# Optimization experiments

Measured on AMD Instinct MI355X. Metric: run time of the kernel, lower is better.

The kernel has to match this reference:

```python
import jax, jax.numpy as jnp
import numpy as np

B, S, H, NH = 2, 2048, 1024, 16


def setup_inputs() -> dict:
    key = jax.random.key(0)
    ks = jax.random.split(key, 5)
    x = jax.random.normal(ks[0], (B, S, H), dtype=jnp.float32)
    # causal mask: True = attend
    mask = jnp.tril(jnp.ones((S, S), dtype=bool))[None, None, :, :]
    scale = 1.0 / np.sqrt(H)
    Wq = jax.random.normal(ks[1], (H, H), dtype=jnp.float32) * scale
    Wk = jax.random.normal(ks[2], (H, H), dtype=jnp.float32) * scale
    Wv = jax.random.normal(ks[3], (H, H), dtype=jnp.float32) * scale
    Wo = jax.random.normal(ks[4], (H, H), dtype=jnp.float32) * scale
    return {"x": x, "mask": mask, "Wq": Wq, "Wk": Wk, "Wv": Wv, "Wo": Wo}


def _split_heads(t, n_heads):
    b, s, h = t.shape
    return t.reshape(b, s, n_heads, h // n_heads).transpose(0, 2, 1, 3)  # (b,h,s,d)


def reference(x, mask, Wq, Wk, Wv, Wo):
    q = _split_heads(x @ Wq, NH)
    k = _split_heads(x @ Wk, NH)
    v = _split_heads(x @ Wv, NH)
    d_head = q.shape[-1]
    scores = jnp.einsum('bhqd,bhkd->bhqk', q, k) / jnp.sqrt(jnp.asarray(d_head, q.dtype))
    neg = jnp.asarray(jnp.finfo(scores.dtype).min, scores.dtype)
    scores = jnp.where(mask, scores, neg)  # mask_to_bias: True->0 bias, False->-inf
    attn = jax.nn.softmax(scores, axis=-1)
    out = jnp.einsum('bhqk,bhkd->bhqd', attn, v)
    out = out.transpose(0, 2, 1, 3).reshape(x.shape[0], x.shape[1], -1)  # merge heads
    return out @ Wo
```

## Files before the change

kernel.cpp:

```cpp
#include <hip/hip_runtime.h>

using u16 = unsigned short;
typedef __attribute__((ext_vector_type(8))) __bf16 bf16x8;
typedef __attribute__((ext_vector_type(4))) float f32x4;
typedef __attribute__((ext_vector_type(8))) u16 u16x8;
typedef __attribute__((ext_vector_type(4))) u16 u16x4;
typedef __attribute__((ext_vector_type(4))) float floatx4;

__device__ __forceinline__ u16 f2bf(float f) {
    union { float f; unsigned u; } x; x.f = f;
    unsigned r = x.u + 0x7fffu + ((x.u >> 16) & 1u);
    return (u16)(r >> 16);
}

__device__ __forceinline__ void gload16(const void* g, void* l) {
    __builtin_amdgcn_global_load_lds((const __attribute__((address_space(1))) void*)g,
                                     (__attribute__((address_space(3))) void*)l, 16, 0, 0);
}

constexpr int Hdim = 1024, Bdim = 2, Sdim = 2048, Dh = 64;
constexpr int NTOK = Bdim * Sdim;

__global__ void cast_x_kernel(const float* __restrict__ x, u16* __restrict__ xb, int n4) {
    int i = blockIdx.x * blockDim.x + threadIdx.x;
    int stride = gridDim.x * blockDim.x;
    for (; i < n4; i += stride) {
        floatx4 v = reinterpret_cast<const floatx4*>(x)[i];
        u16x4 o;
        #pragma unroll
        for (int j = 0; j < 4; ++j) o[j] = f2bf(v[j]);
        reinterpret_cast<u16x4*>(xb)[i] = o;
    }
}

__global__ void transpose_cast_w(const float* __restrict__ W0, const float* __restrict__ W1,
                                 const float* __restrict__ W2, const float* __restrict__ W3,
                                 u16* __restrict__ T0, u16* __restrict__ T1,
                                 u16* __restrict__ T2, u16* __restrict__ T3) {
    __shared__ float tile[32][33];
    const float* W; u16* T;
    switch (blockIdx.z) {
        case 0: W = W0; T = T0; break;
        case 1: W = W1; T = T1; break;
        case 2: W = W2; T = T2; break;
        default: W = W3; T = T3; break;
    }
    int bx = blockIdx.x * 32, by = blockIdx.y * 32;
    int tx = threadIdx.x, ty = threadIdx.y;
    #pragma unroll
    for (int i = 0; i < 4; ++i)
        tile[ty + i * 8][tx] = W[(size_t)(by + ty + i * 8) * Hdim + bx + tx];
    __syncthreads();
    #pragma unroll
    for (int i = 0; i < 4; ++i)
        T[(size_t)(bx + ty + i * 8) * Hdim + by + tx] = f2bf(tile[tx][ty + i * 8]);
}

template <int MODE, int BN>
__global__ __launch_bounds__(256) void gemm_bt(const u16* __restrict__ A, const u16* __restrict__ Bt,
                                               void* __restrict__ C0, void* __restrict__ C1,
                                               void* __restrict__ C2, int N, int K) {
    constexpr int NB = BN / 32;
    __shared__ __align__(16) u16 As[128 * 32];
    __shared__ __align__(16) u16 Bs[BN * 32];
    const int tid = threadIdx.x;
    const int lane = tid & 63, wid = tid >> 6;
    const int wr = wid >> 1, wc = wid & 1;
    const int fr = lane & 15, g = lane >> 4, k8 = g * 8;
    const int rowBase = blockIdx.y * 128, colBase = blockIdx.x * BN;
    const int sr = lane >> 2, sc = (lane & 3) * 8;
    f32x4 acc[4][NB] = {};
    for (int k0 = 0; k0 < K; k0 += 32) {
        __syncthreads();
        #pragma unroll
        for (int i = 0; i < 2; ++i) {
            const int rb = wid * 32 + i * 16;
            gload16(&A[(size_t)(rowBase + rb + sr) * K + k0 + sc], &As[rb * 32]);
        }
        if constexpr (BN == 128) {
            #pragma unroll
            for (int i = 0; i < 2; ++i) {
                const int rb = wid * 32 + i * 16;
                gload16(&Bt[(size_t)(colBase + rb + sr) * K + k0 + sc], &Bs[rb * 32]);
            }
        } else {
            const int rb = wid * 16;
            gload16(&Bt[(size_t)(colBase + rb + sr) * K + k0 + sc], &Bs[rb * 32]);
        }
        __syncthreads();
        bf16x8 af[4], bfr[NB];
        #pragma unroll
        for (int m = 0; m < 4; ++m)
            af[m] = *reinterpret_cast<const bf16x8*>(&As[(wr * 64 + m * 16 + fr) * 32 + k8]);
        #pragma unroll
        for (int n = 0; n < NB; ++n)
            bfr[n] = *reinterpret_cast<const bf16x8*>(&Bs[(wc * (BN / 2) + n * 16 + fr) * 32 + k8]);
        #pragma unroll
        for (int m = 0; m < 4; ++m)
            #pragma unroll
            for (int n = 0; n < NB; ++n)
                acc[m][n] = __builtin_amdgcn_mfma_f32_16x16x32_bf16(af[m], bfr[n], acc[m][n], 0, 0, 0);
    }
    #pragma unroll
    for (int m = 0; m < 4; ++m) {
        #pragma unroll
        for (int n = 0; n < NB; ++n) {
            const int row = rowBase + wr * 64 + m * 16 + g * 4;
            const int col = colBase + wc * (BN / 2) + n * 16 + fr;
            if constexpr (MODE == 0) {
                u16* C = (u16*)C0;
                #pragma unroll
                for (int j = 0; j < 4; ++j) C[(size_t)(row + j) * N + col] = f2bf(acc[m][n][j]);
            } else if constexpr (MODE == 1) {
                float* C = (float*)C0;
                #pragma unroll
                for (int j = 0; j < 4; ++j) C[(size_t)(row + j) * N + col] = acc[m][n][j];
            } else {
                if (col < 1024) {
                    u16* Qm = (u16*)C0;
                    #pragma unroll
                    for (int j = 0; j < 4; ++j) Qm[(size_t)(row + j) * 1024 + col] = f2bf(acc[m][n][j]);
                } else if (col < 2048) {
                    u16* Km = (u16*)C1;
                    #pragma unroll
                    for (int j = 0; j < 4; ++j) Km[(size_t)(row + j) * 1024 + (col - 1024)] = f2bf(acc[m][n][j]);
                } else {
                    u16* Vt = (u16*)C2;
                    u16x4 pk;
                    #pragma unroll
                    for (int j = 0; j < 4; ++j) pk[j] = f2bf(acc[m][n][j]);
                    *reinterpret_cast<u16x4*>(&Vt[(size_t)(col - 2048) * NTOK + row]) = pk;
                }
            }
        }
    }
}

__global__ __launch_bounds__(256, 2) void attn_kernel(const u16* __restrict__ Q, const u16* __restrict__ Km,
                                                      const u16* __restrict__ VtG, u16* __restrict__ AO) {
    __shared__ __align__(16) u16 Kt[2][64 * 64];
    __shared__ __align__(16) u16 Vt[2][64 * 64];
    __shared__ __align__(16) u16 Pw[4][32][72];
    const int tid = threadIdx.x, lane = tid & 63, w = tid >> 6;
    const int bid = blockIdx.x;
    const int xg = bid & 7, rem = bid >> 3;
    const int p = rem & 15, yg = rem >> 4;
    const int grp = xg + 8 * yg;
    const int h = grp & 15, b = grp >> 4;
    const int qsel[2] = { p, 31 - p };
    const int h0 = h * Dh;
    const size_t boff = (size_t)b * Sdim * Hdim;
    const u16* Qb = Q + boff;
    u16* AOb = AO + boff;
    const int fr = lane & 15, g = lane >> 4;

    const int lr = lane >> 3;
    const int lc8 = ((lane & 7) ^ lr) * 8;
    const u16* Kg = Km + boff + (size_t)(w * 8 + lr) * Hdim + h0 + lc8;
    const u16* Vg = VtG + (size_t)(h0 + w * 8 + lr) * NTOK + (size_t)b * Sdim + lc8;

    auto stage = [&](int t, int bufi) {
        const int kv0 = t * 64;
        #pragma unroll
        for (int i = 0; i < 2; ++i) {
            gload16(Kg + (size_t)(kv0 + i * 32) * Hdim, &Kt[bufi][w * 512 + i * 2048]);
            gload16(Vg + (size_t)(i * 32) * NTOK + kv0, &Vt[bufi][w * 512 + i * 2048]);
        }
    };

    constexpr float QSCALE = 0.125f * 1.44269504089f;
    bf16x8 qf[2][2];
    int qrow0[2];
    #pragma unroll
    for (int m = 0; m < 2; ++m) {
        qrow0[m] = qsel[m] * 64 + w * 16;
        #pragma unroll
        for (int c = 0; c < 2; ++c) {
            bf16x8 t = *reinterpret_cast<const bf16x8*>(
                &Qb[(size_t)(qrow0[m] + fr) * Hdim + h0 + c * 32 + g * 8]);
            bf16x8 r;
            #pragma unroll
            for (int j = 0; j < 8; ++j) r[j] = (__bf16)((float)t[j] * QSCALE);
            qf[m][c] = r;
        }
    }

    f32x4 o[2][4] = {};
    float mrow[2][4], lrow[2][4];
    #pragma unroll
    for (int m = 0; m < 2; ++m)
        #pragma unroll
        for (int j = 0; j < 4; ++j) { mrow[m][j] = -INFINITY; lrow[m][j] = 0.f; }

    const int ntiles = qsel[1] + 1;
    stage(0, 0);
    __syncthreads();
    int buf = 0;
    for (int t = 0; t < ntiles; ++t) {
        if (t + 1 < ntiles) stage(t + 1, buf ^ 1);
        const int kv0 = t * 64;
        #pragma unroll
        for (int m = 0; m < 2; ++m) {
            if (t > qsel[m]) continue;
            const bool masked = (t == qsel[m]);
            f32x4 s[4];
            __builtin_amdgcn_s_setprio(1);
            #pragma unroll
            for (int n = 0; n < 4; ++n) {
                const int row = n * 16 + fr;
                const int sw = (row & 7) << 3;
                const u16* kp = &Kt[buf][row * 64];
                bf16x8 kf0 = *reinterpret_cast<const bf16x8*>(&kp[(g * 8) ^ sw]);
                bf16x8 kf1 = *reinterpret_cast<const bf16x8*>(&kp[(32 + g * 8) ^ sw]);
                f32x4 z = {};
                z = __builtin_amdgcn_mfma_f32_16x16x32_bf16(qf[m][0], kf0, z, 0, 0, 0);
                s[n] = __builtin_amdgcn_mfma_f32_16x16x32_bf16(qf[m][1], kf1, z, 0, 0, 0);
            }
            __builtin_amdgcn_s_setprio(0);
            #pragma unroll
            for (int j = 0; j < 4; ++j) {
                const int qrow = qrow0[m] + g * 4 + j;
                float mx = -3.0e38f;
                #pragma unroll
                for (int n = 0; n < 4; ++n) {
                    float v = s[n][j];
                    if (masked) {
                        int kv = kv0 + n * 16 + fr;
                        v = (kv <= qrow) ? v : -3.0e38f;
                        s[n][j] = v;
                    }
                    mx = fmaxf(mx, v);
                }
                #pragma unroll
                for (int off = 1; off < 16; off <<= 1) mx = fmaxf(mx, __shfl_xor(mx, off));
                const float mnew = fmaxf(mrow[m][j], mx);
                const float alpha = exp2f(mrow[m][j] - mnew);
                float rs = 0.f;
                #pragma unroll
                for (int n = 0; n < 4; ++n) {
                    float pv = exp2f(s[n][j] - mnew);
                    rs += pv;
                    Pw[w][m * 16 + g * 4 + j][n * 16 + fr] = f2bf(pv);
                }
                #pragma unroll
                for (int off = 1; off < 16; off <<= 1) rs += __shfl_xor(rs, off);
                lrow[m][j] = lrow[m][j] * alpha + rs;
                mrow[m][j] = mnew;
                #pragma unroll
                for (int n = 0; n < 4; ++n) o[m][n][j] *= alpha;
            }
            bf16x8 pa0 = *reinterpret_cast<const bf16x8*>(&Pw[w][m * 16 + fr][g * 8]);
            bf16x8 pa1 = *reinterpret_cast<const bf16x8*>(&Pw[w][m * 16 + fr][32 + g * 8]);
            __builtin_amdgcn_s_setprio(1);
            #pragma unroll
            for (int n = 0; n < 4; ++n) {
                const int row = n * 16 + fr;
                const int sw = (row & 7) << 3;
                const u16* vp = &Vt[buf][row * 64];
                bf16x8 vf0 = *reinterpret_cast<const bf16x8*>(&vp[(g * 8) ^ sw]);
                bf16x8 vf1 = *reinterpret_cast<const bf16x8*>(&vp[(32 + g * 8) ^ sw]);
                o[m][n] = __builtin_amdgcn_mfma_f32_16x16x32_bf16(pa0, vf0, o[m][n], 0, 0, 0);
                o[m][n] = __builtin_amdgcn_mfma_f32_16x16x32_bf16(pa1, vf1, o[m][n], 0, 0, 0);
            }
            __builtin_amdgcn_s_setprio(0);
        }
        __syncthreads();
        buf ^= 1;
    }

    #pragma unroll
    for (int m = 0; m < 2; ++m) {
        float invl[4];
        #pragma unroll
        for (int j = 0; j < 4; ++j) invl[j] = 1.0f / lrow[m][j];
        #pragma unroll
        for (int n = 0; n < 4; ++n)
            #pragma unroll
            for (int j = 0; j < 4; ++j) {
                int qrow = qrow0[m] + g * 4 + j;
                AOb[(size_t)qrow * Hdim + h0 + n * 16 + fr] = f2bf(o[m][n][j] * invl[j]);
            }
    }
}

extern "C" void kernel_launch(void* const* d_in, const int* in_sizes, int n_in,
                              void* d_out, int out_size, void* d_ws, size_t ws_size,
                              hipStream_t stream) {
    const float* x  = (const float*)d_in[0];
    const float* Wq = (const float*)d_in[2];
    const float* Wk = (const float*)d_in[3];
    const float* Wv = (const float*)d_in[4];
    const float* Wo = (const float*)d_in[5];
    float* out = (float*)d_out;

    u16* ws  = (u16*)d_ws;
    u16* Xb  = ws;
    u16* WqT = ws  + 4194304;
    u16* WkT = WqT + 1048576;
    u16* WvT = WkT + 1048576;
    u16* WoT = WvT + 1048576;
    u16* Qm  = WoT + 1048576;
    u16* Km  = Qm  + 4194304;
    u16* Vt  = Km  + 4194304;
    u16* AO  = Vt  + 4194304;

    cast_x_kernel<<<2048, 256, 0, stream>>>(x, Xb, NTOK * Hdim / 4);
    transpose_cast_w<<<dim3(32, 32, 4), dim3(32, 8), 0, stream>>>(Wq, Wk, Wv, Wo, WqT, WkT, WvT, WoT);
    gemm_bt<2, 128><<<dim3(24, 32), 256, 0, stream>>>(Xb, WqT, Qm, Km, Vt, 3072, Hdim);
    attn_kernel<<<dim3(512), 256, 0, stream>>>(Qm, Km, Vt, AO);
    gemm_bt<1, 64><<<dim3(16, 32), 256, 0, stream>>>(AO, WoT, out, nullptr, nullptr, Hdim, Hdim);
}
```

Measured before the change: 231.5 us.

## Retile attention to one q-tile per block, deepen GEMM K-step, lazy softmax rescale

The attention kernel now gives each block a single 64-row query tile instead of a balanced pair, doubling the grid to 1024 blocks, raising the occupancy hint to 3 and shrinking the P scratch buffer. It also skips the online-softmax rescale when the new row max stays within a threshold of the old one. The GEMM loads 64-wide K slices per barrier instead of 32, halving synchronisation count, and bf16 conversion switches to the compiler cast. Risks include causal load imbalance from dropping the paired tiles, larger LDS use in the GEMM, and the lazy rescale letting exponentials exceed one before normalisation.

```diff
diff --git a/kernel.cpp b/kernel.cpp
--- a/kernel.cpp
+++ b/kernel.cpp
@@ -7,10 +7,9 @@
 typedef __attribute__((ext_vector_type(4))) u16 u16x4;
 typedef __attribute__((ext_vector_type(4))) float floatx4;
 
-__device__ __forceinline__ u16 f2bf(float f) {
-    union { float f; unsigned u; } x; x.f = f;
-    unsigned r = x.u + 0x7fffu + ((x.u >> 16) & 1u);
-    return (u16)(r >> 16);
+__device__ __forceinline__ u16 f2b(float f) {
+    __bf16 h = (__bf16)f;
+    return __builtin_bit_cast(u16, h);
 }
 
 __device__ __forceinline__ void gload16(const void* g, void* l) {
@@ -28,7 +27,7 @@
         floatx4 v = reinterpret_cast<const floatx4*>(x)[i];
         u16x4 o;
         #pragma unroll
-        for (int j = 0; j < 4; ++j) o[j] = f2bf(v[j]);
+        for (int j = 0; j < 4; ++j) o[j] = f2b(v[j]);
         reinterpret_cast<u16x4*>(xb)[i] = o;
     }
 }
@@ -53,7 +52,7 @@
     __syncthreads();
     #pragma unroll
     for (int i = 0; i < 4; ++i)
-        T[(size_t)(bx + ty + i * 8) * Hdim + by + tx] = f2bf(tile[tx][ty + i * 8]);
+        T[(size_t)(bx + ty + i * 8) * Hdim + by + tx] = f2b(tile[tx][ty + i * 8]);
 }
 
 template <int MODE, int BN>
@@ -61,45 +60,43 @@
                                                void* __restrict__ C0, void* __restrict__ C1,
                                                void* __restrict__ C2, int N, int K) {
     constexpr int NB = BN / 32;
-    __shared__ __align__(16) u16 As[128 * 32];
-    __shared__ __align__(16) u16 Bs[BN * 32];
+    __shared__ __align__(16) u16 As[128 * 64];
+    __shared__ __align__(16) u16 Bs[BN * 64];
     const int tid = threadIdx.x;
     const int lane = tid & 63, wid = tid >> 6;
     const int wr = wid >> 1, wc = wid & 1;
-    const int fr = lane & 15, g = lane >> 4, k8 = g * 8;
+    const int fr = lane & 15, g = lane >> 4;
     const int rowBase = blockIdx.y * 128, colBase = blockIdx.x * BN;
-    const int sr = lane >> 2, sc = (lane & 3) * 8;
+    const int sr = lane >> 3, sc = (lane & 7) * 8;
     f32x4 acc[4][NB] = {};
-    for (int k0 = 0; k0 < K; k0 += 32) {
+    for (int k0 = 0; k0 < K; k0 += 64) {
         __syncthreads();
         #pragma unroll
-        for (int i = 0; i < 2; ++i) {
-            const int rb = wid * 32 + i * 16;
-            gload16(&A[(size_t)(rowBase + rb + sr) * K + k0 + sc], &As[rb * 32]);
-        }
-        if constexpr (BN == 128) {
-            #pragma unroll
-            for (int i = 0; i < 2; ++i) {
-                const int rb = wid * 32 + i * 16;
-                gload16(&Bt[(size_t)(colBase + rb + sr) * K + k0 + sc], &Bs[rb * 32]);
-            }
-        } else {
-            const int rb = wid * 16;
-            gload16(&Bt[(size_t)(colBase + rb + sr) * K + k0 + sc], &Bs[rb * 32]);
+        for (int i = 0; i < 4; ++i) {
+            const int rb = i * 32 + wid * 8;
+            gload16(&A[(size_t)(rowBase + rb + sr) * K + k0 + sc], &As[rb * 64]);
+        }
+        #pragma unroll
+        for (int i = 0; i < BN / 32; ++i) {
+            const int rb = i * 32 + wid * 8;
+            gload16(&Bt[(size_t)(colBase + rb + sr) * K + k0 + sc], &Bs[rb * 64]);
         }
         __syncthreads();
-        bf16x8 af[4], bfr[NB];
-        #pragma unroll
-        for (int m = 0; m < 4; ++m)
-            af[m] = *reinterpret_cast<const bf16x8*>(&As[(wr * 64 + m * 16 + fr) * 32 + k8]);
-        #pragma unroll
-        for (int n = 0; n < NB; ++n)
-            bfr[n] = *reinterpret_cast<const bf16x8*>(&Bs[(wc * (BN / 2) + n * 16 + fr) * 32 + k8]);
-        #pragma unroll
-        for (int m = 0; m < 4; ++m)
+        #pragma unroll
+        for (int kk = 0; kk < 2; ++kk) {
+            bf16x8 af[4], bfr[NB];
+            #pragma unroll
+            for (int m = 0; m < 4; ++m)
+                af[m] = *reinterpret_cast<const bf16x8*>(&As[(wr * 64 + m * 16 + fr) * 64 + kk * 32 + g * 8]);
             #pragma unroll
             for (int n = 0; n < NB; ++n)
-                acc[m][n] = __builtin_amdgcn_mfma_f32_16x16x32_bf16(af[m], bfr[n], acc[m][n], 0, 0, 0);
+                bfr[n] = *reinterpret_cast<const bf16x8*>(&Bs[(wc * (BN / 2) + n * 16 + fr) * 64 + kk * 32 + g * 8]);
+            #pragma unroll
+            for (int m = 0; m < 4; ++m)
+                #pragma unroll
+                for (int n = 0; n < NB; ++n)
+                    acc[m][n] = __builtin_amdgcn_mfma_f32_16x16x32_bf16(af[m], bfr[n], acc[m][n], 0, 0, 0);
+        }
     }
     #pragma unroll
     for (int m = 0; m < 4; ++m) {
@@ -110,7 +107,7 @@
             if constexpr (MODE == 0) {
                 u16* C = (u16*)C0;
                 #pragma unroll
-                for (int j = 0; j < 4; ++j) C[(size_t)(row + j) * N + col] = f2bf(acc[m][n][j]);
+                for (int j = 0; j < 4; ++j) C[(size_t)(row + j) * N + col] = f2b(acc[m][n][j]);
             } else if constexpr (MODE == 1) {
                 float* C = (float*)C0;
                 #pragma unroll
@@ -119,16 +116,16 @@
                 if (col < 1024) {
                     u16* Qm = (u16*)C0;
                     #pragma unroll
-                    for (int j = 0; j < 4; ++j) Qm[(size_t)(row + j) * 1024 + col] = f2bf(acc[m][n][j]);
+                    for (int j = 0; j < 4; ++j) Qm[(size_t)(row + j) * 1024 + col] = f2b(acc[m][n][j]);
                 } else if (col < 2048) {
                     u16* Km = (u16*)C1;
                     #pragma unroll
-                    for (int j = 0; j < 4; ++j) Km[(size_t)(row + j) * 1024 + (col - 1024)] = f2bf(acc[m][n][j]);
+                    for (int j = 0; j < 4; ++j) Km[(size_t)(row + j) * 1024 + (col - 1024)] = f2b(acc[m][n][j]);
                 } else {
                     u16* Vt = (u16*)C2;
                     u16x4 pk;
                     #pragma unroll
-                    for (int j = 0; j < 4; ++j) pk[j] = f2bf(acc[m][n][j]);
+                    for (int j = 0; j < 4; ++j) pk[j] = f2b(acc[m][n][j]);
                     *reinterpret_cast<u16x4*>(&Vt[(size_t)(col - 2048) * NTOK + row]) = pk;
                 }
             }
@@ -136,23 +133,24 @@
     }
 }
 
-__global__ __launch_bounds__(256, 2) void attn_kernel(const u16* __restrict__ Q, const u16* __restrict__ Km,
+__global__ __launch_bounds__(256, 3) void attn_kernel(const u16* __restrict__ Q, const u16* __restrict__ Km,
                                                       const u16* __restrict__ VtG, u16* __restrict__ AO) {
     __shared__ __align__(16) u16 Kt[2][64 * 64];
     __shared__ __align__(16) u16 Vt[2][64 * 64];
-    __shared__ __align__(16) u16 Pw[4][32][72];
+    __shared__ __align__(16) u16 Pw[4][16][72];
     const int tid = threadIdx.x, lane = tid & 63, w = tid >> 6;
     const int bid = blockIdx.x;
     const int xg = bid & 7, rem = bid >> 3;
-    const int p = rem & 15, yg = rem >> 4;
+    const int qi = rem & 31, yg = rem >> 5;
     const int grp = xg + 8 * yg;
     const int h = grp & 15, b = grp >> 4;
-    const int qsel[2] = { p, 31 - p };
+    const int qb = 31 - qi;
     const int h0 = h * Dh;
     const size_t boff = (size_t)b * Sdim * Hdim;
     const u16* Qb = Q + boff;
     u16* AOb = AO + boff;
     const int fr = lane & 15, g = lane >> 4;
+    const int qrow0 = qb * 64 + w * 16;
 
     const int lr = lane >> 3;
     const int lc8 = ((lane & 7) ^ lr) * 8;
@@ -169,118 +167,109 @@
     };
 
     constexpr float QSCALE = 0.125f * 1.44269504089f;
-    bf16x8 qf[2][2];
-    int qrow0[2];
-    #pragma unroll
-    for (int m = 0; m < 2; ++m) {
-        qrow0[m] = qsel[m] * 64 + w * 16;
-        #pragma unroll
-        for (int c = 0; c < 2; ++c) {
-            bf16x8 t = *reinterpret_cast<const bf16x8*>(
-                &Qb[(size_t)(qrow0[m] + fr) * Hdim + h0 + c * 32 + g * 8]);
-            bf16x8 r;
-            #pragma unroll
-            for (int j = 0; j < 8; ++j) r[j] = (__bf16)((float)t[j] * QSCALE);
-            qf[m][c] = r;
-        }
-    }
-
-    f32x4 o[2][4] = {};
-    float mrow[2][4], lrow[2][4];
-    #pragma unroll
-    for (int m = 0; m < 2; ++m)
-        #pragma unroll
-        for (int j = 0; j < 4; ++j) { mrow[m][j] = -INFINITY; lrow[m][j] = 0.f; }
-
-    const int ntiles = qsel[1] + 1;
+    bf16x8 qf[2];
+    #pragma unroll
+    for (int c = 0; c < 2; ++c) {
+        bf16x8 t = *reinterpret_cast<const bf16x8*>(
+            &Qb[(size_t)(qrow0 + fr) * Hdim + h0 + c * 32 + g * 8]);
+        bf16x8 r;
+        #pragma unroll
+        for (int j = 0; j < 8; ++j) r[j] = (__bf16)((float)t[j] * QSCALE);
+        qf[c] = r;
+    }
+
+    f32x4 o[4] = {};
+    float mrow[4], lrow[4];
+    #pragma unroll
+    for (int j = 0; j < 4; ++j) { mrow[j] = -INFINITY; lrow[j] = 0.f; }
+
+    const int ntiles = qb + 1;
     stage(0, 0);
     __syncthreads();
     int buf = 0;
     for (int t = 0; t < ntiles; ++t) {
         if (t + 1 < ntiles) stage(t + 1, buf ^ 1);
         const int kv0 = t * 64;
-        #pragma unroll
-        for (int m = 0; m < 2; ++m) {
-            if (t > qsel[m]) continue;
-            const bool masked = (t == qsel[m]);
-            f32x4 s[4];
-            __builtin_amdgcn_s_setprio(1);
+        const bool masked = (t == qb);
+        f32x4 s[4];
+        __builtin_amdgcn_s_setprio(1);
+        #pragma unroll
+        for (int n = 0; n < 4; ++n) {
+            const int row = n * 16 + fr;
+            const int sw = (row & 7) << 3;
+            const u16* kp = &Kt[buf][row * 64];
+            bf16x8 kf0 = *reinterpret_cast<const bf16x8*>(&kp[(g * 8) ^ sw]);
+            bf16x8 kf1 = *reinterpret_cast<const bf16x8*>(&kp[(32 + g * 8) ^ sw]);
+            f32x4 z = {};
+            z = __builtin_amdgcn_mfma_f32_16x16x32_bf16(qf[0], kf0, z, 0, 0, 0);
+            s[n] = __builtin_amdgcn_mfma_f32_16x16x32_bf16(qf[1], kf1, z, 0, 0, 0);
+        }
+        __builtin_amdgcn_s_setprio(0);
+        #pragma unroll
+        for (int j = 0; j < 4; ++j) {
+            const int qrow = qrow0 + g * 4 + j;
+            float mx = -3.0e38f;
             #pragma unroll
             for (int n = 0; n < 4; ++n) {
-                const int row = n * 16 + fr;
-                const int sw = (row & 7) << 3;
-                const u16* kp = &Kt[buf][row * 64];
-                bf16x8 kf0 = *reinterpret_cast<const bf16x8*>(&kp[(g * 8) ^ sw]);
-                bf16x8 kf1 = *reinterpret_cast<const bf16x8*>(&kp[(32 + g * 8) ^ sw]);
-                f32x4 z = {};
-                z = __builtin_amdgcn_mfma_f32_16x16x32_bf16(qf[m][0], kf0, z, 0, 0, 0);
-                s[n] = __builtin_amdgcn_mfma_f32_16x16x32_bf16(qf[m][1], kf1, z, 0, 0, 0);
+                float v = s[n][j];
+                if (masked) {
+                    int kv = kv0 + n * 16 + fr;
+                    v = (kv <= qrow) ? v : -3.0e38f;
+                    s[n][j] = v;
+                }
+                mx = fmaxf(mx, v);
             }
-            __builtin_amdgcn_s_setprio(0);
-            #pragma unroll
-            for (int j = 0; j < 4; ++j) {
-                const int qrow = qrow0[m] + g * 4 + j;
-                float mx = -3.0e38f;
+            #pragma unroll
+            for (int off = 1; off < 16; off <<= 1) mx = fmaxf(mx, __shfl_xor(mx, off));
+            const bool skip = (__all(mx <= mrow[j] + 8.0f) != 0);
+            const float mnew = skip ? mrow[j] : fmaxf(mrow[j], mx);
+            float rs = 0.f;
+            #pragma unroll
+            for (int n = 0; n < 4; ++n) {
+                float pv = exp2f(s[n][j] - mnew);
+                rs += pv;
+                Pw[w][g * 4 + j][n * 16 + fr] = f2b(pv);
+            }
+            #pragma unroll
+            for (int off = 1; off < 16; off <<= 1) rs += __shfl_xor(rs, off);
+            if (skip) {
+                lrow[j] += rs;
+            } else {
+                const float alpha = exp2f(mrow[j] - mnew);
+                lrow[j] = lrow[j] * alpha + rs;
+                mrow[j] = mnew;
                 #pragma unroll
-                for (int n = 0; n < 4; ++n) {
-                    float v = s[n][j];
-                    if (masked) {
-                        int kv = kv0 + n * 16 + fr;
-                        v = (kv <= qrow) ? v : -3.0e38f;
-                        s[n][j] = v;
-                    }
-                    mx = fmaxf(mx, v);
-                }
-                #pragma unroll
-                for (int off = 1; off < 16; off <<= 1) mx = fmaxf(mx, __shfl_xor(mx, off));
-                const float mnew = fmaxf(mrow[m][j], mx);
-                const float alpha = exp2f(mrow[m][j] - mnew);
-                float rs = 0.f;
-                #pragma unroll
-                for (int n = 0; n < 4; ++n) {
-                    float pv = exp2f(s[n][j] - mnew);
-                    rs += pv;
-                    Pw[w][m * 16 + g * 4 + j][n * 16 + fr] = f2bf(pv);
-                }
-                #pragma unroll
-                for (int off = 1; off < 16; off <<= 1) rs += __shfl_xor(rs, off);
-                lrow[m][j] = lrow[m][j] * alpha + rs;
-                mrow[m][j] = mnew;
-                #pragma unroll
-                for (int n = 0; n < 4; ++n) o[m][n][j] *= alpha;
+                for (int n = 0; n < 4; ++n) o[n][j] *= alpha;
             }
-            bf16x8 pa0 = *reinterpret_cast<const bf16x8*>(&Pw[w][m * 16 + fr][g * 8]);
-            bf16x8 pa1 = *reinterpret_cast<const bf16x8*>(&Pw[w][m * 16 + fr][32 + g * 8]);
-            __builtin_amdgcn_s_setprio(1);
-            #pragma unroll
-            for (int n = 0; n < 4; ++n) {
-                const int row = n * 16 + fr;
-                const int sw = (row & 7) << 3;
-                const u16* vp = &Vt[buf][row * 64];
-                bf16x8 vf0 = *reinterpret_cast<const bf16x8*>(&vp[(g * 8) ^ sw]);
-                bf16x8 vf1 = *reinterpret_cast<const bf16x8*>(&vp[(32 + g * 8) ^ sw]);
-                o[m][n] = __builtin_amdgcn_mfma_f32_16x16x32_bf16(pa0, vf0, o[m][n], 0, 0, 0);
-                o[m][n] = __builtin_amdgcn_mfma_f32_16x16x32_bf16(pa1, vf1, o[m][n], 0, 0, 0);
-            }
-            __builtin_amdgcn_s_setprio(0);
-        }
+        }
+        bf16x8 pa0 = *reinterpret_cast<const bf16x8*>(&Pw[w][fr][g * 8]);
+        bf16x8 pa1 = *reinterpret_cast<const bf16x8*>(&Pw[w][fr][32 + g * 8]);
+        __builtin_amdgcn_s_setprio(1);
+        #pragma unroll
+        for (int n = 0; n < 4; ++n) {
+            const int row = n * 16 + fr;
+            const int sw = (row & 7) << 3;
+            const u16* vp = &Vt[buf][row * 64];
+            bf16x8 vf0 = *reinterpret_cast<const bf16x8*>(&vp[(g * 8) ^ sw]);
+            bf16x8 vf1 = *reinterpret_cast<const bf16x8*>(&vp[(32 + g * 8) ^ sw]);
+            o[n] = __builtin_amdgcn_mfma_f32_16x16x32_bf16(pa0, vf0, o[n], 0, 0, 0);
+            o[n] = __builtin_amdgcn_mfma_f32_16x16x32_bf16(pa1, vf1, o[n], 0, 0, 0);
+        }
+        __builtin_amdgcn_s_setprio(0);
         __syncthreads();
         buf ^= 1;
     }
 
-    #pragma unroll
-    for (int m = 0; m < 2; ++m) {
-        float invl[4];
-        #pragma unroll
-        for (int j = 0; j < 4; ++j) invl[j] = 1.0f / lrow[m][j];
-        #pragma unroll
-        for (int n = 0; n < 4; ++n)
-            #pragma unroll
-            for (int j = 0; j < 4; ++j) {
-                int qrow = qrow0[m] + g * 4 + j;
-                AOb[(size_t)qrow * Hdim + h0 + n * 16 + fr] = f2bf(o[m][n][j] * invl[j]);
-            }
-    }
+    float invl[4];
+    #pragma unroll
+    for (int j = 0; j < 4; ++j) invl[j] = 1.0f / lrow[j];
+    #pragma unroll
+    for (int n = 0; n < 4; ++n)
+        #pragma unroll
+        for (int j = 0; j < 4; ++j) {
+            int qrow = qrow0 + g * 4 + j;
+            AOb[(size_t)qrow * Hdim + h0 + n * 16 + fr] = f2b(o[n][j] * invl[j]);
+        }
 }
 
 extern "C" void kernel_launch(void* const* d_in, const int* in_sizes, int n_in,
@@ -307,6 +296,6 @@
     cast_x_kernel<<<2048, 256, 0, stream>>>(x, Xb, NTOK * Hdim / 4);
     transpose_cast_w<<<dim3(32, 32, 4), dim3(32, 8), 0, stream>>>(Wq, Wk, Wv, Wo, WqT, WkT, WvT, WoT);
     gemm_bt<2, 128><<<dim3(24, 32), 256, 0, stream>>>(Xb, WqT, Qm, Km, Vt, 3072, Hdim);
-    attn_kernel<<<dim3(512), 256, 0, stream>>>(Qm, Km, Vt, AO);
+    attn_kernel<<<dim3(1024), 256, 0, stream>>>(Qm, Km, Vt, AO);
     gemm_bt<1, 64><<<dim3(16, 32), 256, 0, stream>>>(AO, WoT, out, nullptr, nullptr, Hdim, Hdim);
 }
```

New measurement: 315.2 us. 1.36x slower.
